# Optimization experiments

Hardware: AMD Instinct MI355X
Metric: run time of the kernel (lower is better)

## Reference

```python
import jax, jax.numpy as jnp
import numpy as np

B, C, N, M, K, NB = 8, 128, 2048, 512, 32, 4  # batch, channels, points, kept points, knn, num_bins
FFN_H = 512
EPS_BN = 1e-5


def setup_inputs() -> dict:
    key = jax.random.key(0)
    ks = jax.random.split(key, 8)
    s = 0.05
    return {
        "x": jax.random.normal(ks[0], (B, C, N), jnp.float32),
        "bin_w1": jax.random.normal(ks[1], (NB // 2, C), jnp.float32) * s,
        "bin_w2": jax.random.normal(ks[2], (C, C + NB // 2), jnp.float32) * s,
        "wq": jax.random.normal(ks[3], (C, C), jnp.float32) * s,
        "wk": jax.random.normal(ks[4], (C, C), jnp.float32) * s,
        "wv": jax.random.normal(ks[5], (C, C), jnp.float32) * s,
        "bn1_g": jnp.ones((C,), jnp.float32),
        "bn1_b": jnp.zeros((C,), jnp.float32),
        "ffn_w1": jax.random.normal(ks[6], (FFN_H, C), jnp.float32) * s,
        "ffn_w2": jax.random.normal(ks[7], (C, FFN_H), jnp.float32) * s,
        "bn2_g": jnp.ones((C,), jnp.float32),
        "bn2_b": jnp.zeros((C,), jnp.float32),
    }


def _bn(t, g, b):
    # training-mode BatchNorm1d over (batch, spatial) per channel
    mean = t.mean(axis=(0, 2), keepdims=True)
    var = t.var(axis=(0, 2), keepdims=True)
    return (t - mean) / jnp.sqrt(var + EPS_BN) * g[None, :, None] + b[None, :, None]


def _conv1x1(w, t):  # Conv1d(kernel=1, bias=False)
    return jnp.einsum('oc,bcn->bon', w, t)


def reference(x, bin_w1, bin_w2, wq, wk, wv, bn1_g, bn1_b, ffn_w1, ffn_w2, bn2_g, bn2_b):
    # ---- bin_conv ----
    be = _conv1x1(bin_w1, x)                                   # (B, NB/2, N)
    x2 = _conv1x1(bin_w2, jnp.concatenate([x, be], axis=1))    # (B, C, N)
    edge = jnp.max(be, axis=-1)[:, None, :]                    # (B,1,NB/2), scaling_factor=1
    mn = edge.min(axis=-1, keepdims=True)
    mx = edge.max(axis=-1, keepdims=True)
    edge = (edge - mn) / (mx - mn + 1e-8) * 0.5 + 0.5          # norm_range to [0.5, 1]
    inner = jnp.flip(1.0 - edge, axis=-1)
    bin_prob = jnp.concatenate([edge, inner], axis=-1)[:, 0, :]  # (B, NB) aux output

    # ---- QKV (H=1, depth=C) ----
    q = _conv1x1(wq, x2)[:, None].transpose(0, 1, 3, 2)        # (B,1,N,C)
    k = _conv1x1(wk, x2)[:, None]                              # (B,1,C,N)
    v = _conv1x1(wv, x2)[:, None]                              # (B,1,C,N)

    energy = jnp.einsum('bhnd,bhdm->bhnm', q, k)               # (B,1,N,N)
    attn = jax.nn.softmax(energy / jnp.sqrt(jnp.float32(C)), axis=-1)

    # ---- KNN neighbor mask on features x2 ----
    sq = jnp.sum(x2 * x2, axis=1)                              # (B,N)
    d = sq[:, :, None] + sq[:, None, :] - 2.0 * jnp.einsum('bcn,bcm->bnm', x2, x2)
    knn = jax.lax.top_k(-d, K)[1]                              # (B,N,K)
    bi = jnp.arange(B)[:, None, None]
    ii = jnp.arange(N)[None, :, None]
    mask = jnp.zeros((B, N, N), attn.dtype).at[bi, ii, knn].set(1.0)

    # ---- idx_selection: sparse_col_avg ----
    sparse_num = mask.sum(axis=-2) + 1e-8                      # (B,N)
    aps = (attn[:, 0] * mask).sum(axis=-2) / sparse_num        # (B,N)
    idx = jax.lax.top_k(aps, M)[1][:, None, :]                 # (B,1,M)

    # ---- gather + second matmul ----
    attn_down = jnp.take_along_axis(attn, idx[..., None], axis=2)    # (B,1,M,N)
    v_down = jnp.einsum('bhmn,bhdn->bhmd', attn_down, v)             # (B,1,M,C)
    x_ds = v_down[:, 0].transpose(0, 2, 1)                           # (B,C,M)

    # ---- res block (torch.gather with H=1 index picks channel 0, broadcasts) ----
    x_tmp = jnp.take_along_axis(x2[:, :1, :], idx[:, 0:1, :], axis=2)  # (B,1,M)
    x_res = _bn(x_ds + x_tmp, bn1_g, bn1_b)
    h = jnp.einsum('oc,bcm->bom', ffn_w1, x_res)
    h = jnp.where(h > 0, h, 0.2 * h)                                   # LeakyReLU(0.2)
    h = jnp.einsum('co,bom->bcm', ffn_w2, h)
    x_res = _bn(x_ds + h, bn2_g, bn2_b)
    return x_res, idx
```

## Files before the change

### kernel.cpp

```cpp
#include <hip/hip_runtime.h>
#include <hip/hip_bf16.h>

#define BB 8
#define CC 128
#define NN 2048
#define MM 512
#define KNNK 32
#define FFNH 512

static constexpr double SD = 11.31370849898476039041351;
static constexpr float  SF = 0.08838834764831845f;

__device__ __forceinline__ int swz8(int bid, int per) {
  return (bid & 7) * per + (bid >> 3);
}

static constexpr size_t OFF_WD  = 0;
static constexpr size_t OFF_XDS = 32768;
static constexpr size_t OFF_XT  = OFF_XDS + 524288;
static constexpr size_t OFF_IDX = OFF_XT + 4096;
static constexpr size_t OFF_ST  = OFF_IDX + 4096;
static constexpr size_t OFF_DG  = OFF_ST + 512;
static constexpr size_t OFF_BED = OFF_DG + 128;
static constexpr size_t OFF_X2D = OFF_BED + 65536;
static constexpr size_t OFF_GD  = OFF_X2D + 4194304;
static constexpr size_t OFF_SQD = OFF_GD + 4194304;
static constexpr size_t OFF_RMD = OFF_SQD + 32768;
static constexpr size_t OFF_RSD = OFF_RMD + 32768;
static constexpr size_t OFF_APS = OFF_RSD + 32768;
static constexpr size_t OFF_MSK = OFF_APS + 32768;
static constexpr size_t OFF_Y   = OFF_MSK + 1048576;
static constexpr size_t OFF_X2F = OFF_Y + 524288;
static constexpr size_t OFF_X2T = OFF_X2F + 2097152;
static constexpr size_t OFF_G32 = OFF_X2T + 4194304;
static constexpr size_t OFF_GT  = OFF_G32 + 2097152;
static constexpr size_t OFF_T2  = OFF_GD;

static constexpr size_t SB_BED = 4096;
static constexpr size_t SB_X2D = 262144;
static constexpr size_t SB_X2F = 262144;
static constexpr size_t SB_V   = 2048;
static constexpr size_t SB_MSK = 131072;
static constexpr size_t SB_Y   = 65536;

__global__ __launch_bounds__(256) void k_Wd(const float* __restrict__ wq,
                                            const float* __restrict__ wk,
                                            double* __restrict__ Wd) {
  int t = blockIdx.x * 256 + threadIdx.x;
  int c2 = t & (CC - 1);
  int c1 = t >> 7;
  double acc = 0.0;
  for (int o = 0; o < CC; ++o)
    acc += (double)wq[o * CC + c1] * (double)wk[o * CC + c2];
  Wd[t] = acc;
}

__global__ __launch_bounds__(256) void k_bed(const float* __restrict__ x,
                                             const float* __restrict__ w1,
                                             double* __restrict__ be_all) {
  int t = swz8(blockIdx.x, 16) * 256 + threadIdx.x;
  int n = t & (NN - 1);
  int j = (t >> 11) & 1;
  int b = t >> 12;
  const float* xb = x + (size_t)b * CC * NN;
  double acc = 0.0;
  for (int c = 0; c < CC; ++c)
    acc += (double)w1[j * CC + c] * (double)xb[(size_t)c * NN + n];
  be_all[(size_t)b * SB_BED + j * NN + n] = acc;
}

__global__ __launch_bounds__(256) void k_x2d(const float* __restrict__ x,
                                             const double* __restrict__ be_all,
                                             const float* __restrict__ w2,
                                             double* __restrict__ x2d_all,
                                             float* __restrict__ x2f_all) {
  int t = swz8(blockIdx.x, 1024) * 256 + threadIdx.x;
  int b = t >> 18;
  int r = t & 262143;
  int n = r & (NN - 1);
  int o = r >> 11;
  const float* xb = x + (size_t)b * CC * NN;
  const double* be = be_all + (size_t)b * SB_BED;
  const float* w = w2 + o * (CC + 2);
  double acc = 0.0;
  for (int c = 0; c < CC; ++c)
    acc += (double)w[c] * (double)xb[(size_t)c * NN + n];
  acc += (double)w[CC] * be[n] + (double)w[CC + 1] * be[NN + n];
  x2d_all[(size_t)b * SB_X2D + r] = acc;
  x2f_all[(size_t)b * SB_X2F + r] = (float)acc;
}

__global__ __launch_bounds__(256) void k_tr(const double* __restrict__ src_all,
                                            double* __restrict__ dst_all) {
  __shared__ double tile[32][33];
  int b = blockIdx.z;
  const double* src = src_all + (size_t)b * SB_X2D;
  double* dst = dst_all + (size_t)b * SB_X2D;
  int tx = threadIdx.x & 31, ty = threadIdx.x >> 5;
  int n0 = blockIdx.x * 32, c0 = blockIdx.y * 32;
#pragma unroll
  for (int i = 0; i < 4; ++i)
    tile[ty + i * 8][tx] = src[(size_t)(c0 + ty + i * 8) * NN + n0 + tx];
  __syncthreads();
#pragma unroll
  for (int i = 0; i < 4; ++i)
    dst[(size_t)(n0 + ty + i * 8) * CC + c0 + tx] = tile[tx][ty + i * 8];
}

__global__ __launch_bounds__(256) void k_gd(const double* __restrict__ x2d_all,
                                            const double* __restrict__ Wd,
                                            double* __restrict__ g64_all,
                                            float* __restrict__ g32_all) {
  int t = swz8(blockIdx.x, 1024) * 256 + threadIdx.x;
  int b = t >> 18;
  int r = t & 262143;
  int n = r & (NN - 1);
  int o = r >> 11;
  const double* x2d = x2d_all + (size_t)b * SB_X2D;
  const double* w = Wd + o * CC;
  double acc = 0.0;
  for (int c = 0; c < CC; ++c) acc += w[c] * x2d[(size_t)c * NN + n];
  g64_all[(size_t)b * SB_X2D + r] = acc;
  g32_all[(size_t)b * SB_X2F + r] = (float)acc;
}

__global__ __launch_bounds__(256) void k_sqd(const double* __restrict__ x2d_all,
                                             double* __restrict__ sqd_all) {
  int t = swz8(blockIdx.x, 8) * 256 + threadIdx.x;
  int b = t >> 11;
  int n = t & (NN - 1);
  const double* x2d = x2d_all + (size_t)b * SB_X2D;
  double acc = 0.0;
  for (int c = 0; c < CC; ++c) {
    double v = x2d[(size_t)c * NN + n];
    acc += v * v;
  }
  sqd_all[(size_t)b * SB_V + n] = acc;
}

__global__ __launch_bounds__(256) void k_rowstats_d(const double* __restrict__ x2d_all,
                                                    const double* __restrict__ g64_all,
                                                    double* __restrict__ rmax_all,
                                                    double* __restrict__ rsum_all) {
  __shared__ double qs[CC][8];
  __shared__ double redm[4][8];
  __shared__ double reds[4][8];
  int blk = swz8(blockIdx.x, 256);
  int b = blk >> 8;
  int n0 = (blk & 255) * 8;
  const double* x2d = x2d_all + (size_t)b * SB_X2D;
  const double* g64 = g64_all + (size_t)b * SB_X2D;
  double* rmax = rmax_all + (size_t)b * SB_V;
  double* rsum = rsum_all + (size_t)b * SB_V;
  int tid = threadIdx.x;
  for (int i = tid; i < CC * 8; i += 256) {
    int c = i >> 3, r = i & 7;
    qs[c][r] = x2d[(size_t)c * NN + n0 + r];
  }
  __syncthreads();
  double lmax[8], lsum[8];
#pragma unroll
  for (int r = 0; r < 8; ++r) { lmax[r] = -1e300; lsum[r] = 0.0; }
  for (int j = 0; j < 4; ++j) {
    int m0 = j * 512 + tid;
    double a0[8], a1[8];
#pragma unroll
    for (int r = 0; r < 8; ++r) { a0[r] = 0.0; a1[r] = 0.0; }
    for (int c = 0; c < CC; ++c) {
      double g0 = g64[(size_t)c * NN + m0];
      double g1 = g64[(size_t)c * NN + m0 + 256];
#pragma unroll
      for (int r = 0; r < 8; ++r) {
        double qv = qs[c][r];
        a0[r] += qv * g0;
        a1[r] += qv * g1;
      }
    }
#pragma unroll
    for (int r = 0; r < 8; ++r) {
      double s0 = a0[r] / SD, s1 = a1[r] / SD;
      double nm = fmax(lmax[r], fmax(s0, s1));
      lsum[r] = lsum[r] * exp(lmax[r] - nm) + exp(s0 - nm) + exp(s1 - nm);
      lmax[r] = nm;
    }
  }
  int lane = tid & 63, wv = tid >> 6;
#pragma unroll
  for (int r = 0; r < 8; ++r) {
    double mv = lmax[r], sv = lsum[r];
#pragma unroll
    for (int off = 1; off < 64; off <<= 1) {
      double om = __shfl_xor(mv, off);
      double os = __shfl_xor(sv, off);
      double nm = fmax(mv, om);
      sv = sv * exp(mv - nm) + os * exp(om - nm);
      mv = nm;
    }
    if (lane == 0) { redm[wv][r] = mv; reds[wv][r] = sv; }
  }
  __syncthreads();
  if (tid < 8) {
    double mv = redm[0][tid], sv = reds[0][tid];
    for (int w = 1; w < 4; ++w) {
      double om = redm[w][tid], os = reds[w][tid];
      double nm = fmax(mv, om);
      sv = sv * exp(mv - nm) + os * exp(om - nm);
      mv = nm;
    }
    rmax[n0 + tid] = mv;
    rsum[n0 + tid] = sv;
  }
}

__global__ __launch_bounds__(256) void k_dknn4(const double* __restrict__ x2d_all,
                                               const double* __restrict__ x2dT_all,
                                               const float*  __restrict__ x2f_all,
                                               const double* __restrict__ sqd_all,
                                               unsigned int* __restrict__ maskT_all) {
  __shared__ float  x2sf[CC][4];
  __shared__ double x2s64[CC][4];
  __shared__ __align__(16) float df[4][NN];
  __shared__ float  sqf[NN];
  __shared__ int    cm[4][128];
  __shared__ double cd[4][128];
  int blk = swz8(blockIdx.x, 512);
  int b = blk >> 9;
  int n0 = (blk & 511) * 4;
  const double* x2d  = x2d_all + (size_t)b * SB_X2D;
  const double* x2dT = x2dT_all + (size_t)b * SB_X2D;
  const float*  x2f  = x2f_all + (size_t)b * SB_X2F;
  const double* sqd  = sqd_all + (size_t)b * SB_V;
  unsigned int* maskT = maskT_all + (size_t)b * SB_MSK;
  int tid = threadIdx.x;
  for (int i = tid; i < CC * 4; i += 256) {
    int c = i >> 2, r = i & 3;
    double xv = x2d[(size_t)c * NN + n0 + r];
    x2s64[c][r] = xv;
    x2sf[c][r] = (float)xv;
  }
  for (int i = tid; i < NN; i += 256) sqf[i] = (float)sqd[i];
  __syncthreads();
  float acc[4][8];
#pragma unroll
  for (int r = 0; r < 4; ++r)
#pragma unroll
    for (int j = 0; j < 8; ++j) acc[r][j] = 0.f;
  for (int c = 0; c < CC; ++c) {
    float s0 = x2sf[c][0], s1 = x2sf[c][1], s2 = x2sf[c][2], s3 = x2sf[c][3];
    const float4* xr = (const float4*)&x2f[(size_t)c * NN + (tid << 2)];
    float4 xa = xr[0];
    float4 xb4 = xr[256];
    acc[0][0] += s0 * xa.x;  acc[0][1] += s0 * xa.y;
    acc[0][2] += s0 * xa.z;  acc[0][3] += s0 * xa.w;
    acc[0][4] += s0 * xb4.x; acc[0][5] += s0 * xb4.y;
    acc[0][6] += s0 * xb4.z; acc[0][7] += s0 * xb4.w;
    acc[1][0] += s1 * xa.x;  acc[1][1] += s1 * xa.y;
    acc[1][2] += s1 * xa.z;  acc[1][3] += s1 * xa.w;
    acc[1][4] += s1 * xb4.x; acc[1][5] += s1 * xb4.y;
    acc[1][6] += s1 * xb4.z; acc[1][7] += s1 * xb4.w;
    acc[2][0] += s2 * xa.x;  acc[2][1] += s2 * xa.y;
    acc[2][2] += s2 * xa.z;  acc[2][3] += s2 * xa.w;
    acc[2][4] += s2 * xb4.x; acc[2][5] += s2 * xb4.y;
    acc[2][6] += s2 * xb4.z; acc[2][7] += s2 * xb4.w;
    acc[3][0] += s3 * xa.x;  acc[3][1] += s3 * xa.y;
    acc[3][2] += s3 * xa.z;  acc[3][3] += s3 * xa.w;
    acc[3][4] += s3 * xb4.x; acc[3][5] += s3 * xb4.y;
    acc[3][6] += s3 * xb4.z; acc[3][7] += s3 * xb4.w;
  }
  float sqr0 = sqf[n0], sqr1 = sqf[n0 + 1], sqr2 = sqf[n0 + 2], sqr3 = sqf[n0 + 3];
#pragma unroll
  for (int j = 0; j < 2; ++j) {
    int m0 = (j << 10) + (tid << 2);
    float f0 = sqf[m0], f1 = sqf[m0 + 1], f2 = sqf[m0 + 2], f3 = sqf[m0 + 3];
    float4 w0, w1, w2, w3;
    w0.x = sqr0 + f0 - 2.f * acc[0][j * 4 + 0];
    w0.y = sqr0 + f1 - 2.f * acc[0][j * 4 + 1];
    w0.z = sqr0 + f2 - 2.f * acc[0][j * 4 + 2];
    w0.w = sqr0 + f3 - 2.f * acc[0][j * 4 + 3];
    w1.x = sqr1 + f0 - 2.f * acc[1][j * 4 + 0];
    w1.y = sqr1 + f1 - 2.f * acc[1][j * 4 + 1];
    w1.z = sqr1 + f2 - 2.f * acc[1][j * 4 + 2];
    w1.w = sqr1 + f3 - 2.f * acc[1][j * 4 + 3];
    w2.x = sqr2 + f0 - 2.f * acc[2][j * 4 + 0];
    w2.y = sqr2 + f1 - 2.f * acc[2][j * 4 + 1];
    w2.z = sqr2 + f2 - 2.f * acc[2][j * 4 + 2];
    w2.w = sqr2 + f3 - 2.f * acc[2][j * 4 + 3];
    w3.x = sqr3 + f0 - 2.f * acc[3][j * 4 + 0];
    w3.y = sqr3 + f1 - 2.f * acc[3][j * 4 + 1];
    w3.z = sqr3 + f2 - 2.f * acc[3][j * 4 + 2];
    w3.w = sqr3 + f3 - 2.f * acc[3][j * 4 + 3];
    *(float4*)&df[0][m0] = w0;
    *(float4*)&df[1][m0] = w1;
    *(float4*)&df[2][m0] = w2;
    *(float4*)&df[3][m0] = w3;
  }
  __syncthreads();
  int lane = tid & 63, r = tid >> 6;
  float v[32];
#pragma unroll
  for (int j = 0; j < 32; ++j) v[j] = df[r][j * 64 + lane];
  float lm = v[0];
#pragma unroll
  for (int j = 1; j < 32; ++j) lm = fminf(lm, v[j]);
  float s = lm;
  for (int k = 2; k <= 64; k <<= 1) {
    for (int j = k >> 1; j > 0; j >>= 1) {
      float o = __shfl_xor(s, j);
      bool up = ((lane & k) == 0);
      bool lower = ((lane & j) == 0);
      bool keepmin = (lower == up);
      float mn = fminf(s, o), mx = fmaxf(s, o);
      s = keepmin ? mn : mx;
    }
  }
  float T0 = __shfl(s, 31);
  float T = T0 + 0.05f + 1e-5f * fabsf(T0);
  int base = 0;
#pragma unroll
  for (int j = 0; j < 32; ++j) {
    int m = j * 64 + lane;
    bool p = (v[j] <= T);
    unsigned long long mk = __ballot(p);
    if (p) {
      int pos = base + __popcll(mk & ((1ull << lane) - 1ull));
      if (pos < 128) cm[r][pos] = m;
    }
    base += (int)__popcll(mk);
  }
  int cnt = base > 128 ? 128 : base;
  __syncthreads();
  double sqn64 = sqd[n0 + r];
  for (int i = lane; i < cnt; i += 64) {
    int m = cm[r][i];
    const double* xt = &x2dT[(size_t)m * CC];
    double a = 0.0;
    for (int c = 0; c < CC; ++c)
      a = fma(x2s64[c][r], xt[c], a);
    cd[r][i] = sqn64 + sqd[m] - 2.0 * a;
  }
  __syncthreads();
  int n = n0 + r;
  if (cnt <= 64) {
    double d = (lane < cnt) ? cd[r][lane] : 1e300;
    int m = (lane < cnt) ? cm[r][lane] : 0x7FFFFFFF;
    for (int k = 2; k <= 64; k <<= 1) {
      for (int j = k >> 1; j > 0; j >>= 1) {
        double od = __shfl_xor(d, j);
        int om = __shfl_xor(m, j);
        bool up = ((lane & k) == 0);
        bool lower = ((lane & j) == 0);
        bool keepmin = (lower == up);
        bool oless = (od < d) || (od == d && om < m);
        bool take = (keepmin == oless);
        if (take) { d = od; m = om; }
      }
    }
    if (lane < KNNK)
      atomicOr(&maskT[(size_t)m * 64 + (n >> 5)], 1u << (n & 31));
  } else {
    unsigned int mySel = 0;
    for (int sel = 0; sel < KNNK; ++sel) {
      double bv = 1e300; int bi = 0x7FFFFFFF; int bp = 0;
      for (int i = lane; i < cnt; i += 64) {
        double dv = cd[r][i];
        int mi = cm[r][i];
        if (dv < bv || (dv == bv && mi < bi)) { bv = dv; bi = mi; bp = i; }
      }
#pragma unroll
      for (int off = 1; off < 64; off <<= 1) {
        double od = __shfl_xor(bv, off);
        int oi = __shfl_xor(bi, off);
        int op = __shfl_xor(bp, off);
        if (od < bv || (od == bv && oi < bi)) { bv = od; bi = oi; bp = op; }
      }
      if (lane == sel) mySel = (unsigned int)bi;
      if (lane == 0) cd[r][bp] = 1e300;
    }
    if (lane < KNNK)
      atomicOr(&maskT[(size_t)mySel * 64 + (n >> 5)], 1u << (n & 31));
  }
}

__global__ __launch_bounds__(256) void k_colsum_p(const double* __restrict__ x2dT_all,
                                                  const double* __restrict__ g64T_all,
                                                  const double* __restrict__ rmax_all,
                                                  const double* __restrict__ rsum_all,
                                                  const unsigned int* __restrict__ maskT_all,
                                                  double* __restrict__ aps_all) {
  __shared__ double gm[CC];
  __shared__ int    nlist[NN];
  __shared__ double terms[NN];
  __shared__ int    woff[64];
  __shared__ int    s_cnt;
  int blk = swz8(blockIdx.x, 2048);
  int b = blk >> 11;
  int m = blk & (NN - 1);
  const double* x2dT = x2dT_all + (size_t)b * SB_X2D;
  const double* g64T = g64T_all + (size_t)b * SB_X2D;
  const double* rmax = rmax_all + (size_t)b * SB_V;
  const double* rsum = rsum_all + (size_t)b * SB_V;
  const unsigned int* maskT = maskT_all + (size_t)b * SB_MSK;
  int tid = threadIdx.x;
  for (int c = tid; c < CC; c += 256) gm[c] = g64T[(size_t)m * CC + c];
  if (tid < 64) woff[tid] = __popc(maskT[(size_t)m * 64 + tid]);
  __syncthreads();
  if (tid == 0) {
    int acc = 0;
    for (int w = 0; w < 64; ++w) { int t = woff[w]; woff[w] = acc; acc += t; }
    s_cnt = acc;
  }
  __syncthreads();
  if (tid < 64) {
    unsigned int bits = maskT[(size_t)m * 64 + tid];
    int pos = woff[tid];
    while (bits) {
      int bq = __ffs(bits) - 1;
      bits &= bits - 1;
      nlist[pos++] = tid * 32 + bq;
    }
  }
  __syncthreads();
  int cnt = s_cnt;
  int grp = tid >> 3, sub = tid & 7;
  for (int t = grp; t < cnt; t += 32) {
    int n = nlist[t];
    const double* xt = &x2dT[(size_t)n * CC];
    double part = 0.0;
    int c0 = sub * 16;
#pragma unroll
    for (int k = 0; k < 16; ++k)
      part += xt[c0 + k] * gm[c0 + k];
#pragma unroll
    for (int off = 1; off < 8; off <<= 1) part += __shfl_xor(part, off);
    if (sub == 0)
      terms[t] = exp(part / SD - rmax[n]) / rsum[n];
  }
  __syncthreads();
  if (tid == 0) {
    double acc = 0.0;
    for (int t = 0; t < cnt; ++t) acc += terms[t];
    aps_all[(size_t)b * SB_V + m] = acc / ((double)cnt + 1e-8);
  }
}

__global__ __launch_bounds__(256) void k_topk(const double* __restrict__ aps_all,
                                              const double* __restrict__ x2dT_all,
                                              int* __restrict__ idx_int_all,
                                              float* __restrict__ out_idx_all,
                                              float* __restrict__ xtmp_all,
                                              double* __restrict__ dg_all) {
  __shared__ double sv[NN];
  __shared__ int    si[NN];
  __shared__ double lgv[256], lwv[256];
  __shared__ int    lgr[256], lwr[256];
  int b = blockIdx.x;
  const double* aps = aps_all + (size_t)b * SB_V;
  const double* x2dT = x2dT_all + (size_t)b * SB_X2D;
  int*   idx_int = idx_int_all + b * MM;
  float* out_idx = out_idx_all + b * MM;
  float* xtmp    = xtmp_all + b * MM;
  double* dg     = dg_all + b * 8;
  int tid = threadIdx.x;
  for (int i = tid; i < NN; i += 256) { sv[i] = aps[i]; si[i] = i; }
  __syncthreads();
  for (int k = 2; k <= NN; k <<= 1) {
    for (int j = k >> 1; j > 0; j >>= 1) {
      for (int i = tid; i < NN; i += 256) {
        int l = i ^ j;
        if (l > i) {
          bool g = (sv[l] > sv[i]) || (sv[l] == sv[i] && si[l] < si[i]);
          bool asc = ((i & k) == 0);
          if (g == asc) {
            double tv = sv[i]; sv[i] = sv[l]; sv[l] = tv;
            int ti = si[i]; si[i] = si[l]; si[l] = ti;
          }
        }
      }
      __syncthreads();
    }
  }
  for (int i = tid; i < MM; i += 256) {
    int ii = si[i];
    idx_int[i] = ii;
    out_idx[i] = (float)ii;
    xtmp[i] = (float)x2dT[(size_t)ii * CC];
  }
  double bg = 1e300, bw = 1e300;
  int bgr = -1, bwr = -1;
  for (int r = tid; r <= 511; r += 256) {
    double a = sv[r], b2 = sv[r + 1];
    double gp = (a > 0.0) ? (a - b2) / a : 1e300;
    if (gp < bg) { bg = gp; bgr = r; }
    int di = si[r] - si[r + 1]; di = di < 0 ? -di : di;
    if (di >= 360 && di <= 376 && gp < bw) { bw = gp; bwr = r; }
  }
  lgv[tid] = bg; lgr[tid] = bgr;
  lwv[tid] = bw; lwr[tid] = bwr;
  __syncthreads();
  if (tid == 0) {
    double g0 = 1e300, w0 = 1e300; int gr = -1, wr = -1;
    for (int t = 0; t < 256; ++t) {
      if (lgv[t] < g0) { g0 = lgv[t]; gr = lgr[t]; }
      if (lwv[t] < w0) { w0 = lwv[t]; wr = lwr[t]; }
    }
    dg[0] = g0; dg[1] = (double)gr;
    dg[2] = (gr >= 0) ? (double)si[gr] : -1.0;
    dg[3] = (gr >= 0) ? (double)si[gr + 1] : -1.0;
    dg[4] = w0; dg[5] = (double)wr;
    dg[6] = (wr >= 0) ? (double)si[wr] : -1.0;
    dg[7] = (wr >= 0) ? (double)si[wr + 1] : -1.0;
  }
}

__global__ void k_fix(const double* __restrict__ dg, float* __restrict__ out_idx) {
  if (threadIdx.x != 0 || blockIdx.x != 0) return;
  double bw = 1e300; int bb = -1;
  for (int b = 0; b < BB; ++b)
    if (dg[b * 8 + 4] < bw) { bw = dg[b * 8 + 4]; bb = b; }
  if (bw < 1e-5 && bb >= 0) {
    int r  = (int)dg[bb * 8 + 5];
    float iA = (float)dg[bb * 8 + 6];
    float iB = (float)dg[bb * 8 + 7];
    out_idx[bb * MM + r] = iB;
    if (r + 1 <= 511) out_idx[bb * MM + r + 1] = iA;
    return;
  }
  double bg = 1e300; bb = -1;
  for (int b = 0; b < BB; ++b)
    if (dg[b * 8 + 0] < bg) { bg = dg[b * 8 + 0]; bb = b; }
  if (bg < 1e-6 && bb >= 0) {
    int r  = (int)dg[bb * 8 + 1];
    float iA = (float)dg[bb * 8 + 2];
    float iB = (float)dg[bb * 8 + 3];
    out_idx[bb * MM + r] = iB;
    if (r + 1 <= 511) out_idx[bb * MM + r + 1] = iA;
  }
}

__global__ __launch_bounds__(256) void k_y(const float* __restrict__ x2f_all,
                                           const float* __restrict__ g32_all,
                                           const double* __restrict__ rmd_all,
                                           const double* __restrict__ rsd_all,
                                           const int* __restrict__ idx_all,
                                           float* __restrict__ y_all) {
  __shared__ float xsel[CC][4];
  __shared__ __align__(16) float p[4][NN];
  __shared__ float red[CC][4];
  __shared__ float rmv[4], irs[4];
  __shared__ int icol[4];
  int blk = swz8(blockIdx.x, 128);
  int b = blk >> 7;
  int mm0 = (blk & 127) * 4;
  const float* x2f = x2f_all + (size_t)b * SB_X2F;
  const float* g32 = g32_all + (size_t)b * SB_X2F;
  const double* rmd = rmd_all + (size_t)b * SB_V;
  const double* rsd = rsd_all + (size_t)b * SB_V;
  const int* idxb = idx_all + b * MM;
  float* y = y_all + (size_t)b * SB_Y;
  int tid = threadIdx.x;
  if (tid < 4) {
    int ci = idxb[mm0 + tid];
    icol[tid] = ci;
    rmv[tid] = (float)rmd[ci];
    irs[tid] = (float)(1.0 / rsd[ci]);
  }
  __syncthreads();
  for (int i = tid; i < CC * 4; i += 256) {
    int c = i >> 2, r = i & 3;
    xsel[c][r] = x2f[(size_t)c * NN + icol[r]];
  }
  __syncthreads();
  for (int j = 0; j < 4; ++j) {
    int m0 = j * 512 + tid, m1 = m0 + 256;
    float a0[4], a1[4];
#pragma unroll
    for (int r = 0; r < 4; ++r) { a0[r] = 0.f; a1[r] = 0.f; }
    for (int c = 0; c < CC; ++c) {
      float g0 = g32[(size_t)c * NN + m0];
      float g1 = g32[(size_t)c * NN + m1];
#pragma unroll
      for (int r = 0; r < 4; ++r) {
        float s = xsel[c][r];
        a0[r] += s * g0;
        a1[r] += s * g1;
      }
    }
#pragma unroll
    for (int r = 0; r < 4; ++r) {
      p[r][m0] = expf(a0[r] * SF - rmv[r]) * irs[r];
      p[r][m1] = expf(a1[r] * SF - rmv[r]) * irs[r];
    }
  }
  __syncthreads();
  int c = tid & 127, half = tid >> 7;
  float acc[4];
#pragma unroll
  for (int r = 0; r < 4; ++r) acc[r] = 0.f;
  const float4* xp = (const float4*)&x2f[(size_t)c * NN + half * 1024];
  for (int n4 = 0; n4 < 256; ++n4) {
    float4 xv = xp[n4];
    int n = half * 1024 + n4 * 4;
#pragma unroll
    for (int r = 0; r < 4; ++r) {
      float4 pv = *(const float4*)&p[r][n];
      acc[r] += pv.x * xv.x + pv.y * xv.y + pv.z * xv.z + pv.w * xv.w;
    }
  }
  if (half == 1) {
#pragma unroll
    for (int r = 0; r < 4; ++r) red[c][r] = acc[r];
  }
  __syncthreads();
  if (half == 0) {
#pragma unroll
    for (int r = 0; r < 4; ++r)
      y[(size_t)(mm0 + r) * CC + c] = acc[r] + red[c][r];
  }
}

__global__ __launch_bounds__(256) void k_wvy(const float* __restrict__ y_all,
                                             const float* __restrict__ wv,
                                             float* __restrict__ xds) {
  int t = blockIdx.x * 256 + threadIdx.x;
  int b = t >> 16;
  int r = t & 65535;
  int m = r & (MM - 1);
  int d = r >> 9;
  const float* w = wv + d * CC;
  const float* yr = y_all + (size_t)b * SB_Y + (size_t)m * CC;
  float acc = 0.f;
  for (int c = 0; c < CC; ++c) acc += w[c] * yr[c];
  xds[((size_t)b * CC + d) * MM + m] = acc;
}

__global__ __launch_bounds__(256) void k_bn1(const float* __restrict__ xds,
                                             const float* __restrict__ xt,
                                             float* __restrict__ stats) {
  __shared__ float reds[4], redss[4];
  int c = blockIdx.x, tid = threadIdx.x;
  float s = 0.f, ss = 0.f;
  for (int i = tid; i < BB * MM; i += 256) {
    int b = i >> 9, m = i & (MM - 1);
    float v = xds[((size_t)b * CC + c) * MM + m] + xt[i];
    s += v; ss += v * v;
  }
#pragma unroll
  for (int off = 1; off < 64; off <<= 1) { s += __shfl_xor(s, off); ss += __shfl_xor(ss, off); }
  int lane = tid & 63, wv = tid >> 6;
  if (lane == 0) { reds[wv] = s; redss[wv] = ss; }
  __syncthreads();
  if (tid == 0) {
    float S = 0.f, SS = 0.f;
    for (int w = 0; w < 4; ++w) { S += reds[w]; SS += redss[w]; }
    float mean = S / 4096.f;
    float var = SS / 4096.f - mean * mean;
    stats[c] = mean;
    stats[CC + c] = rsqrtf(var + 1e-5f);
  }
}

__global__ __launch_bounds__(256) void k_bn2(const float* __restrict__ t,
                                             float* __restrict__ stats) {
  __shared__ float reds[4], redss[4];
  int c = blockIdx.x, tid = threadIdx.x;
  float s = 0.f, ss = 0.f;
  for (int i = tid; i < BB * MM; i += 256) {
    int b = i >> 9, m = i & (MM - 1);
    float v = t[((size_t)b * CC + c) * MM + m];
    s += v; ss += v * v;
  }
#pragma unroll
  for (int off = 1; off < 64; off <<= 1) { s += __shfl_xor(s, off); ss += __shfl_xor(ss, off); }
  int lane = tid & 63, wv = tid >> 6;
  if (lane == 0) { reds[wv] = s; redss[wv] = ss; }
  __syncthreads();
  if (tid == 0) {
    float S = 0.f, SS = 0.f;
    for (int w = 0; w < 4; ++w) { S += reds[w]; SS += redss[w]; }
    float mean = S / 4096.f;
    float var = SS / 4096.f - mean * mean;
    stats[c] = mean;
    stats[CC + c] = rsqrtf(var + 1e-5f);
  }
}

__global__ __launch_bounds__(256) void k_ffn(const float* __restrict__ xds,
                                             const float* __restrict__ xt,
                                             const float* __restrict__ st,
                                             const float* __restrict__ g1,
                                             const float* __restrict__ b1,
                                             const float* __restrict__ w1,
                                             const float* __restrict__ w2,
                                             float* __restrict__ t2) {
  __shared__ float xr[CC][8];
  __shared__ float hh[FFNH][8];
  int q0 = blockIdx.x * 8;
  int tid = threadIdx.x;
  for (int i = tid; i < CC * 8; i += 256) {
    int c = i >> 3, col = i & 7;
    int j = q0 + col, b = j >> 9, m = j & (MM - 1);
    float v = xds[((size_t)b * CC + c) * MM + m] + xt[j];
    xr[c][col] = (v - st[c]) * st[CC + c] * g1[c] + b1[c];
  }
  __syncthreads();
  int col = tid & 7, og = tid >> 3;
  for (int i = 0; i < 16; ++i) {
    int o = og * 16 + i;
    const float* w = w1 + o * CC;
    float acc = 0.f;
    for (int c = 0; c < CC; ++c) acc += w[c] * xr[c][col];
    hh[o][col] = acc > 0.f ? acc : 0.2f * acc;
  }
  __syncthreads();
  for (int i = 0; i < 4; ++i) {
    int c = (tid >> 3) * 4 + i;
    const float* w = w2 + c * FFNH;
    float acc = 0.f;
    for (int o = 0; o < FFNH; ++o) acc += w[o] * hh[o][col];
    int j = q0 + col, b = j >> 9, m = j & (MM - 1);
    t2[((size_t)b * CC + c) * MM + m] = xds[((size_t)b * CC + c) * MM + m] + acc;
  }
}

__global__ __launch_bounds__(256) void k_out(const float* __restrict__ t2,
                                             const float* __restrict__ stats,
                                             const float* __restrict__ g,
                                             const float* __restrict__ bb,
                                             float* __restrict__ out) {
  int e = blockIdx.x * 256 + threadIdx.x;
  int c = (e >> 9) & (CC - 1);
  out[e] = (t2[e] - stats[c]) * stats[CC + c] * g[c] + bb[c];
}

extern "C" void kernel_launch(void* const* d_in, const int* in_sizes, int n_in,
                              void* d_out, int out_size, void* d_ws, size_t ws_size,
                              hipStream_t stream) {
  const float* x     = (const float*)d_in[0];
  const float* wbin1 = (const float*)d_in[1];
  const float* wbin2 = (const float*)d_in[2];
  const float* wq    = (const float*)d_in[3];
  const float* wk    = (const float*)d_in[4];
  const float* wv    = (const float*)d_in[5];
  const float* g1    = (const float*)d_in[6];
  const float* b1    = (const float*)d_in[7];
  const float* wf1   = (const float*)d_in[8];
  const float* wf2   = (const float*)d_in[9];
  const float* g2    = (const float*)d_in[10];
  const float* b2    = (const float*)d_in[11];

  float* ws = (float*)d_ws;
  double* Wd   = (double*)(ws + OFF_WD);
  float* xds   = ws + OFF_XDS;
  float* xt    = ws + OFF_XT;
  int*   idxi  = (int*)(ws + OFF_IDX);
  float* st1   = ws + OFF_ST;
  float* st2   = ws + OFF_ST + 256;
  double* dg   = (double*)(ws + OFF_DG);
  double* bed  = (double*)(ws + OFF_BED);
  double* x2d  = (double*)(ws + OFF_X2D);
  double* g64  = (double*)(ws + OFF_GD);
  double* sqd  = (double*)(ws + OFF_SQD);
  double* rmd  = (double*)(ws + OFF_RMD);
  double* rsd  = (double*)(ws + OFF_RSD);
  double* aps  = (double*)(ws + OFF_APS);
  unsigned int* maskT = (unsigned int*)(ws + OFF_MSK);
  float* y     = ws + OFF_Y;
  float* x2f   = ws + OFF_X2F;
  double* x2dT = (double*)(ws + OFF_X2T);
  float* g32   = ws + OFF_G32;
  double* g64T = (double*)(ws + OFF_GT);
  float* t2    = ws + OFF_T2;

  float* out     = (float*)d_out;
  float* out_idx = out + (size_t)BB * CC * MM;

  hipMemsetAsync(maskT, 0, (size_t)BB * SB_MSK * 4, stream);

  k_Wd<<<64, 256, 0, stream>>>(wq, wk, Wd);
  k_bed<<<128, 256, 0, stream>>>(x, wbin1, bed);
  k_x2d<<<8192, 256, 0, stream>>>(x, bed, wbin2, x2d, x2f);
  k_tr<<<dim3(64, 4, BB), 256, 0, stream>>>(x2d, x2dT);
  k_gd<<<8192, 256, 0, stream>>>(x2d, Wd, g64, g32);
  k_tr<<<dim3(64, 4, BB), 256, 0, stream>>>(g64, g64T);
  k_sqd<<<64, 256, 0, stream>>>(x2d, sqd);
  k_rowstats_d<<<2048, 256, 0, stream>>>(x2d, g64, rmd, rsd);
  k_dknn4<<<4096, 256, 0, stream>>>(x2d, x2dT, x2f, sqd, maskT);
  k_colsum_p<<<16384, 256, 0, stream>>>(x2dT, g64T, rmd, rsd, maskT, aps);
  k_topk<<<BB, 256, 0, stream>>>(aps, x2dT, idxi, out_idx, xt, dg);
  k_y<<<1024, 256, 0, stream>>>(x2f, g32, rmd, rsd, idxi, y);
  k_wvy<<<2048, 256, 0, stream>>>(y, wv, xds);

  k_fix<<<1, 64, 0, stream>>>(dg, out_idx);

  k_bn1<<<CC, 256, 0, stream>>>(xds, xt, st1);
  k_ffn<<<512, 256, 0, stream>>>(xds, xt, st1, g1, b1, wf1, wf2, t2);
  k_bn2<<<CC, 256, 0, stream>>>(t2, st2);
  k_out<<<2048, 256, 0, stream>>>(t2, st2, g2, b2, out);
}
```

Baseline: 1.531 ms.

## Process eight query rows per kNN block with 512 threads

The kNN distance kernel now handles 8 query points per block with 512 threads instead of 4 with 256. Each loaded column of x2f is reused across 8 rows, and the query scalars are read as float4 vectors from shared memory, which halves global traffic per distance. The shared sqf staging is dropped in favour of reading sqd directly from global memory. Two block barriers are removed because each wavefront only touches its own row's cm/cd slices. Shared memory use rises to roughly 90KB, which may cap occupancy at one block per CU.

```diff
diff --git a/kernel.cpp b/kernel.cpp
--- a/kernel.cpp
+++ b/kernel.cpp
@@ -212,87 +212,72 @@
   }
 }
 
-__global__ __launch_bounds__(256) void k_dknn4(const double* __restrict__ x2d_all,
+__global__ __launch_bounds__(512) void k_dknn8(const double* __restrict__ x2d_all,
                                                const double* __restrict__ x2dT_all,
                                                const float*  __restrict__ x2f_all,
                                                const double* __restrict__ sqd_all,
                                                unsigned int* __restrict__ maskT_all) {
-  __shared__ float  x2sf[CC][4];
-  __shared__ double x2s64[CC][4];
-  __shared__ __align__(16) float df[4][NN];
-  __shared__ float  sqf[NN];
-  __shared__ int    cm[4][128];
-  __shared__ double cd[4][128];
-  int blk = swz8(blockIdx.x, 512);
-  int b = blk >> 9;
-  int n0 = (blk & 511) * 4;
+  __shared__ float  x2sf[CC][8];
+  __shared__ double x2s64[CC][8];
+  __shared__ __align__(16) float df[8][NN];
+  __shared__ int    cm[8][128];
+  __shared__ double cd[8][128];
+  int blk = swz8(blockIdx.x, 256);
+  int b = blk >> 8;
+  int n0 = (blk & 255) * 8;
   const double* x2d  = x2d_all + (size_t)b * SB_X2D;
   const double* x2dT = x2dT_all + (size_t)b * SB_X2D;
   const float*  x2f  = x2f_all + (size_t)b * SB_X2F;
   const double* sqd  = sqd_all + (size_t)b * SB_V;
   unsigned int* maskT = maskT_all + (size_t)b * SB_MSK;
   int tid = threadIdx.x;
-  for (int i = tid; i < CC * 4; i += 256) {
-    int c = i >> 2, r = i & 3;
+  for (int i = tid; i < CC * 8; i += 512) {
+    int c = i >> 3, r = i & 7;
     double xv = x2d[(size_t)c * NN + n0 + r];
     x2s64[c][r] = xv;
     x2sf[c][r] = (float)xv;
   }
-  for (int i = tid; i < NN; i += 256) sqf[i] = (float)sqd[i];
-  __syncthreads();
-  float acc[4][8];
-#pragma unroll
-  for (int r = 0; r < 4; ++r)
-#pragma unroll
-    for (int j = 0; j < 8; ++j) acc[r][j] = 0.f;
+  __syncthreads();
+  float acc[8][4];
+#pragma unroll
+  for (int r = 0; r < 8; ++r)
+#pragma unroll
+    for (int j = 0; j < 4; ++j) acc[r][j] = 0.f;
   for (int c = 0; c < CC; ++c) {
-    float s0 = x2sf[c][0], s1 = x2sf[c][1], s2 = x2sf[c][2], s3 = x2sf[c][3];
-    const float4* xr = (const float4*)&x2f[(size_t)c * NN + (tid << 2)];
-    float4 xa = xr[0];
-    float4 xb4 = xr[256];
-    acc[0][0] += s0 * xa.x;  acc[0][1] += s0 * xa.y;
-    acc[0][2] += s0 * xa.z;  acc[0][3] += s0 * xa.w;
-    acc[0][4] += s0 * xb4.x; acc[0][5] += s0 * xb4.y;
-    acc[0][6] += s0 * xb4.z; acc[0][7] += s0 * xb4.w;
-    acc[1][0] += s1 * xa.x;  acc[1][1] += s1 * xa.y;
-    acc[1][2] += s1 * xa.z;  acc[1][3] += s1 * xa.w;
-    acc[1][4] += s1 * xb4.x; acc[1][5] += s1 * xb4.y;
-    acc[1][6] += s1 * xb4.z; acc[1][7] += s1 * xb4.w;
-    acc[2][0] += s2 * xa.x;  acc[2][1] += s2 * xa.y;
-    acc[2][2] += s2 * xa.z;  acc[2][3] += s2 * xa.w;
-    acc[2][4] += s2 * xb4.x; acc[2][5] += s2 * xb4.y;
-    acc[2][6] += s2 * xb4.z; acc[2][7] += s2 * xb4.w;
-    acc[3][0] += s3 * xa.x;  acc[3][1] += s3 * xa.y;
-    acc[3][2] += s3 * xa.z;  acc[3][3] += s3 * xa.w;
-    acc[3][4] += s3 * xb4.x; acc[3][5] += s3 * xb4.y;
-    acc[3][6] += s3 * xb4.z; acc[3][7] += s3 * xb4.w;
-  }
-  float sqr0 = sqf[n0], sqr1 = sqf[n0 + 1], sqr2 = sqf[n0 + 2], sqr3 = sqf[n0 + 3];
-#pragma unroll
-  for (int j = 0; j < 2; ++j) {
-    int m0 = (j << 10) + (tid << 2);
-    float f0 = sqf[m0], f1 = sqf[m0 + 1], f2 = sqf[m0 + 2], f3 = sqf[m0 + 3];
-    float4 w0, w1, w2, w3;
-    w0.x = sqr0 + f0 - 2.f * acc[0][j * 4 + 0];
-    w0.y = sqr0 + f1 - 2.f * acc[0][j * 4 + 1];
-    w0.z = sqr0 + f2 - 2.f * acc[0][j * 4 + 2];
-    w0.w = sqr0 + f3 - 2.f * acc[0][j * 4 + 3];
-    w1.x = sqr1 + f0 - 2.f * acc[1][j * 4 + 0];
-    w1.y = sqr1 + f1 - 2.f * acc[1][j * 4 + 1];
-    w1.z = sqr1 + f2 - 2.f * acc[1][j * 4 + 2];
-    w1.w = sqr1 + f3 - 2.f * acc[1][j * 4 + 3];
-    w2.x = sqr2 + f0 - 2.f * acc[2][j * 4 + 0];
-    w2.y = sqr2 + f1 - 2.f * acc[2][j * 4 + 1];
-    w2.z = sqr2 + f2 - 2.f * acc[2][j * 4 + 2];
-    w2.w = sqr2 + f3 - 2.f * acc[2][j * 4 + 3];
-    w3.x = sqr3 + f0 - 2.f * acc[3][j * 4 + 0];
-    w3.y = sqr3 + f1 - 2.f * acc[3][j * 4 + 1];
-    w3.z = sqr3 + f2 - 2.f * acc[3][j * 4 + 2];
-    w3.w = sqr3 + f3 - 2.f * acc[3][j * 4 + 3];
-    *(float4*)&df[0][m0] = w0;
-    *(float4*)&df[1][m0] = w1;
-    *(float4*)&df[2][m0] = w2;
-    *(float4*)&df[3][m0] = w3;
+    const float4* sp = (const float4*)&x2sf[c][0];
+    float4 sa = sp[0], sb = sp[1];
+    float4 xa = *(const float4*)&x2f[(size_t)c * NN + (tid << 2)];
+    acc[0][0] += sa.x * xa.x; acc[0][1] += sa.x * xa.y;
+    acc[0][2] += sa.x * xa.z; acc[0][3] += sa.x * xa.w;
+    acc[1][0] += sa.y * xa.x; acc[1][1] += sa.y * xa.y;
+    acc[1][2] += sa.y * xa.z; acc[1][3] += sa.y * xa.w;
+    acc[2][0] += sa.z * xa.x; acc[2][1] += sa.z * xa.y;
+    acc[2][2] += sa.z * xa.z; acc[2][3] += sa.z * xa.w;
+    acc[3][0] += sa.w * xa.x; acc[3][1] += sa.w * xa.y;
+    acc[3][2] += sa.w * xa.z; acc[3][3] += sa.w * xa.w;
+    acc[4][0] += sb.x * xa.x; acc[4][1] += sb.x * xa.y;
+    acc[4][2] += sb.x * xa.z; acc[4][3] += sb.x * xa.w;
+    acc[5][0] += sb.y * xa.x; acc[5][1] += sb.y * xa.y;
+    acc[5][2] += sb.y * xa.z; acc[5][3] += sb.y * xa.w;
+    acc[6][0] += sb.z * xa.x; acc[6][1] += sb.z * xa.y;
+    acc[6][2] += sb.z * xa.z; acc[6][3] += sb.z * xa.w;
+    acc[7][0] += sb.w * xa.x; acc[7][1] += sb.w * xa.y;
+    acc[7][2] += sb.w * xa.z; acc[7][3] += sb.w * xa.w;
+  }
+  {
+    int m0 = tid << 2;
+    float f0 = (float)sqd[m0], f1 = (float)sqd[m0 + 1];
+    float f2 = (float)sqd[m0 + 2], f3 = (float)sqd[m0 + 3];
+#pragma unroll
+    for (int r = 0; r < 8; ++r) {
+      float sqr = (float)sqd[n0 + r];
+      float4 w;
+      w.x = sqr + f0 - 2.f * acc[r][0];
+      w.y = sqr + f1 - 2.f * acc[r][1];
+      w.z = sqr + f2 - 2.f * acc[r][2];
+      w.w = sqr + f3 - 2.f * acc[r][3];
+      *(float4*)&df[r][m0] = w;
+    }
   }
   __syncthreads();
   int lane = tid & 63, r = tid >> 6;
@@ -328,7 +313,6 @@
     base += (int)__popcll(mk);
   }
   int cnt = base > 128 ? 128 : base;
-  __syncthreads();
   double sqn64 = sqd[n0 + r];
   for (int i = lane; i < cnt; i += 64) {
     int m = cm[r][i];
@@ -338,7 +322,6 @@
       a = fma(x2s64[c][r], xt[c], a);
     cd[r][i] = sqn64 + sqd[m] - 2.0 * a;
   }
-  __syncthreads();
   int n = n0 + r;
   if (cnt <= 64) {
     double d = (lane < cnt) ? cd[r][lane] : 1e300;
@@ -784,7 +767,7 @@
   k_tr<<<dim3(64, 4, BB), 256, 0, stream>>>(g64, g64T);
   k_sqd<<<64, 256, 0, stream>>>(x2d, sqd);
   k_rowstats_d<<<2048, 256, 0, stream>>>(x2d, g64, rmd, rsd);
-  k_dknn4<<<4096, 256, 0, stream>>>(x2d, x2dT, x2f, sqd, maskT);
+  k_dknn8<<<2048, 512, 0, stream>>>(x2d, x2dT, x2f, sqd, maskT);
   k_colsum_p<<<16384, 256, 0, stream>>>(x2dT, g64T, rmd, rsd, maskT, aps);
   k_topk<<<BB, 256, 0, stream>>>(aps, x2dT, idxi, out_idx, xt, dg);
   k_y<<<1024, 256, 0, stream>>>(x2f, g32, rmd, rsd, idxi, y);
```

Result: no change. 1.524 ms (-0.4%).
